# Performance work log

Measured on AMD Instinct MI355X. Metric: run time of the kernel, lower is better.

Reference implementation:

```python
import jax, jax.numpy as jnp
import numpy as np

N_LEVELS = 16
F_PER_LEVEL = 2
LOG2_T = 19
T = 1 << LOG2_T            # 524288 entries per level
BASE_RES = 16
PER_LEVEL_SCALE = 1.3819
HIDDEN = 64
DIM = 3
PRIMES = (1, 2654435761, 805459861)  # tcnn spatial hash primes

# 8 corner offsets of the unit cube, shape (8, 3)
_CORNERS = np.stack(np.meshgrid(*([np.array([0, 1])] * DIM), indexing='ij'), -1).reshape(-1, DIM)


def hashgrid_encode(x01, table):
    """x01: (N,3) in [0,1]; table: (L, T, F). Returns (N, L*F)."""
    offs = jnp.asarray(_CORNERS, dtype=jnp.int32)          # (8,3)
    offs_u = offs.astype(jnp.uint32)
    feats = []
    for lvl in range(N_LEVELS):
        scale = BASE_RES * (PER_LEVEL_SCALE ** lvl) - 1.0   # grid scale (tcnn convention)
        res = int(np.ceil(scale)) + 1                       # grid resolution for this level
        pos = x01 * jnp.float32(scale) + 0.5
        p0 = jnp.floor(pos)
        w = pos - p0                                        # (N,3) trilinear weights
        p0i = p0.astype(jnp.int32)
        corner = p0i[:, None, :] + offs[None]               # (N,8,3)
        if res ** DIM <= T:
            # dense (coarse) level: linear indexing
            idx = corner[..., 0] + corner[..., 1] * res + corner[..., 2] * (res * res)
        else:
            # fine level: xor spatial hash modulo table size
            c = p0i[:, None, :].astype(jnp.uint32) + offs_u[None]
            h = (c[..., 0] * jnp.uint32(PRIMES[0])) ^ (c[..., 1] * jnp.uint32(PRIMES[1])) ^ (c[..., 2] * jnp.uint32(PRIMES[2]))
            idx = (h & jnp.uint32(T - 1)).astype(jnp.int32)
        cf = table[lvl][idx]                                # (N,8,F) irregular gather
        # trilinear weight per corner: prod over dims of (w if offset==1 else 1-w)
        wmask = jnp.where(offs[None] == 1, w[:, None, :], 1.0 - w[:, None, :])  # (N,8,3)
        wc = jnp.prod(wmask, axis=-1)                       # (N,8)
        feats.append(jnp.sum(cf * wc[..., None], axis=1))   # (N,F)
    return jnp.concatenate(feats, axis=-1)                  # (N, 32)


def _xavier(key, fan_in, fan_out):
    lim = jnp.sqrt(6.0 / (fan_in + fan_out))
    return jax.random.uniform(key, (fan_in, fan_out), jnp.float32, -lim, lim)


def setup_inputs() -> dict:
    key = jax.random.key(0)
    k = jax.random.split(key, 8)
    x = jax.random.uniform(k[0], (1048576, DIM), jnp.float32, -1.0, 1.0)
    # tcnn hashgrid init: uniform(-1e-4, 1e-4)
    table = jax.random.uniform(k[1], (N_LEVELS, T, F_PER_LEVEL), jnp.float32, -1e-4, 1e-4)
    in_dim = N_LEVELS * F_PER_LEVEL
    W1 = _xavier(k[2], in_dim, HIDDEN); b1 = jnp.zeros((HIDDEN,), jnp.float32)
    W2 = _xavier(k[3], HIDDEN, HIDDEN); b2 = jnp.zeros((HIDDEN,), jnp.float32)
    W3 = _xavier(k[4], HIDDEN, 1);      b3 = jnp.zeros((1,), jnp.float32)
    return {"x": x, "table": table, "W1": W1, "b1": b1, "W2": W2, "b2": b2, "W3": W3, "b3": b3}


def reference(x, table, W1, b1, W2, b2, W3, b3):
    x01 = (x + 1.0) * 0.5                       # map [-1,1] -> [0,1]
    enc = hashgrid_encode(x01, table)           # (N, 32)
    h = jax.nn.relu(enc @ W1 + b1)
    h = jax.nn.relu(h @ W2 + b2)
    h = h @ W3 + b3                             # (N, 1), clip_sdf is None
    return h
```

## Files before the change

kernel.cpp:

```cpp
#include <hip/hip_runtime.h>
#include <hip/hip_fp16.h>
#include <cstdint>

#define NTHREADS 256
#define TBL_SIZE (1u << 19)
#define HIDDEN 64
#define NLVL 16
#define NDENSE 5
#define NHASH (NLVL - NDENSE)
#define PPT 2
#define ENC_SCALE 256.0f
#define ENC_INV (1.0f / 256.0f)

struct Levels { float scale[16]; int res[16]; int dense[16]; };
constexpr Levels make_levels() {
    Levels L{};
    double s = 16.0;
    for (int l = 0; l < 16; ++l) {
        double sc = s - 1.0;
        L.scale[l] = (float)sc;
        int fi = (int)sc;
        int res = fi + (((double)fi < sc) ? 1 : 0) + 1;
        L.res[l] = res;
        L.dense[l] = ((long long)res * res * res <= (long long)TBL_SIZE) ? 1 : 0;
        s *= 1.3819;
    }
    return L;
}
constexpr Levels LV = make_levels();
static_assert(LV.dense[NDENSE - 1] == 1 && LV.dense[NDENSE] == 0, "dense split");

struct PairOffs { int off[17]; int total; };
constexpr PairOffs make_pairoffs() {
    PairOffs P{}; int o = 0;
    for (int l = 0; l < 16; ++l) {
        P.off[l] = o;
        if (LV.dense[l]) {
            const int r = LV.res[l];
            o += r * (1 + r + r * r) + 2;
        }
    }
    P.off[16] = o; P.total = o;
    return P;
}
constexpr PairOffs PO = make_pairoffs();

#define H16(M) M(0) M(1) M(2) M(3) M(4) M(5) M(6) M(7) \
               M(8) M(9) M(10) M(11) M(12) M(13) M(14) M(15)

typedef _Float16 f16x8 __attribute__((ext_vector_type(8)));
typedef float f32x4 __attribute__((ext_vector_type(4)));

static __device__ __forceinline__ __half2 u32_h2(uint32_t u) {
    union { uint32_t u; __half2 h; } c; c.u = u; return c.h;
}
static __device__ __forceinline__ uint32_t h2_u32(__half2 h) {
    union { __half2 h; uint32_t u; } c; c.h = h; return c.u;
}

__global__ __launch_bounds__(256) void cvt_table(const float2* __restrict__ in,
                                                 __half2* __restrict__ out, int n) {
    for (int i = blockIdx.x * 256 + threadIdx.x; i < n; i += gridDim.x * 256) {
        const float2 v = in[i];
        out[i] = __floats2half2_rn(v.x, v.y);
    }
}

__global__ __launch_bounds__(256) void cvt_quads(const float2* __restrict__ tf,
                                                 uint4* __restrict__ qd) {
    for (int i = blockIdx.x * 256 + threadIdx.x; i < PO.total; i += gridDim.x * 256) {
        int lvl = 0;
        #pragma unroll
        for (int l = 0; l < NLVL; ++l)
            if (LV.dense[l] && i >= PO.off[l] && i < PO.off[l + 1]) lvl = l;
        const int local = i - PO.off[lvl];
        const int res = LV.res[lvl];
        const float2* base = tf + (size_t)lvl * TBL_SIZE + local;
        uint4 q;
        q.x = h2_u32(__floats2half2_rn(base[0].x, base[0].y));
        q.y = h2_u32(__floats2half2_rn(base[1].x, base[1].y));
        q.z = h2_u32(__floats2half2_rn(base[res].x, base[res].y));
        q.w = h2_u32(__floats2half2_rn(base[res + 1].x, base[res + 1].y));
        qd[i] = q;
    }
}

__global__ __launch_bounds__(256) void cvt_wfrags(const float* __restrict__ W1,
                                                  const float* __restrict__ W2,
                                                  __half* __restrict__ w1f,
                                                  __half* __restrict__ w2f) {
    const int t = blockIdx.x * 256 + threadIdx.x;
    for (int i = t; i < 4 * 64 * 8; i += gridDim.x * 256) {
        const int j = i & 7, lane = (i >> 3) & 63, nt = i >> 9;
        const int k = (lane >> 4) * 8 + j;
        const int o = (lane & 15) + 16 * nt;
        w1f[i] = __float2half(W1[k * HIDDEN + o]);
    }
    for (int i = t; i < 4 * 2 * 64 * 8; i += gridDim.x * 256) {
        const int j = i & 7, lane = (i >> 3) & 63, kb = (i >> 9) & 1, nt = i >> 10;
        const int k = 32 * kb + (lane >> 4) * 8 + j;
        const int o = (lane & 15) + 16 * nt;
        w2f[i] = __float2half(W2[k * HIDDEN + o]);
    }
}

static __device__ __forceinline__ float2 gather_dense(
    const uint4* __restrict__ qd, int res, int doff,
    int iu, int iv, int iw, float wu, float wv, float ww)
{
    float f0 = 0.0f, f1 = 0.0f;
    const float lx = 1.0f - wu;
    const int base = iu + iv * res + iw * res * res;
    #pragma unroll
    for (int o2 = 0; o2 < 2; ++o2) {
        const int idx = base + (o2 ? res * res : 0);
        const uint4 q = qd[doff + idx];
        const float2 a = __half22float2(u32_h2(q.x));
        const float2 b = __half22float2(u32_h2(q.y));
        const float2 c = __half22float2(u32_h2(q.z));
        const float2 d = __half22float2(u32_h2(q.w));
        const float x0l = fmaf(lx, a.x, wu * b.x);
        const float x1l = fmaf(lx, c.x, wu * d.x);
        const float y0l = fmaf(lx, a.y, wu * b.y);
        const float y1l = fmaf(lx, c.y, wu * d.y);
        const float bil0 = fmaf(1.0f - wv, x0l, wv * x1l);
        const float bil1 = fmaf(1.0f - wv, y0l, wv * y1l);
        const float wz = o2 ? ww : 1.0f - ww;
        f0 = fmaf(bil0, wz, f0);
        f1 = fmaf(bil1, wz, f1);
    }
    return make_float2(f0, f1);
}

static __device__ __forceinline__ float2 gather_hash(
    const __half2* __restrict__ tl,
    int iu, int iv, int iw, float wu, float wv, float ww)
{
    float f0 = 0.0f, f1 = 0.0f;
    const float lx = 1.0f - wu;
    const uint32_t r1a = (uint32_t)iv * 2654435761u;
    const uint32_t r1b = r1a + 2654435761u;
    const uint32_t r2a = (uint32_t)iw * 805459861u;
    const uint32_t r2b = r2a + 805459861u;
    if ((iu & 1) == 0) {
        #pragma unroll
        for (int b4 = 0; b4 < 4; ++b4) {
            const int o1 = (b4 >> 1) & 1, o2 = b4 & 1;
            const uint32_t rest = (o1 ? r1b : r1a) ^ (o2 ? r2b : r2a);
            const uint32_t h0 = ((uint32_t)iu ^ rest) & (TBL_SIZE - 1u);
            const unsigned long long pr =
                *reinterpret_cast<const unsigned long long*>(tl + (h0 & ~1u));
            const uint32_t lo = (uint32_t)pr, hi = (uint32_t)(pr >> 32);
            const uint32_t sel = h0 & 1u;
            const float2 a = __half22float2(u32_h2(sel ? hi : lo));
            const float2 b = __half22float2(u32_h2(sel ? lo : hi));
            const float wyz = (o1 ? wv : 1.0f - wv) * (o2 ? ww : 1.0f - ww);
            f0 = fmaf(fmaf(lx, a.x, wu * b.x), wyz, f0);
            f1 = fmaf(fmaf(lx, a.y, wu * b.y), wyz, f1);
        }
    } else {
        #pragma unroll
        for (int b4 = 0; b4 < 4; ++b4) {
            const int o1 = (b4 >> 1) & 1, o2 = b4 & 1;
            const uint32_t rest = (o1 ? r1b : r1a) ^ (o2 ? r2b : r2a);
            const uint32_t h0 = ((uint32_t)iu ^ rest) & (TBL_SIZE - 1u);
            const uint32_t h1 = ((uint32_t)(iu + 1) ^ rest) & (TBL_SIZE - 1u);
            const float2 a = __half22float2(tl[h0]);
            const float2 b = __half22float2(tl[h1]);
            const float wyz = (o1 ? wv : 1.0f - wv) * (o2 ? ww : 1.0f - ww);
            f0 = fmaf(fmaf(lx, a.x, wu * b.x), wyz, f0);
            f1 = fmaf(fmaf(lx, a.y, wu * b.y), wyz, f1);
        }
    }
    return make_float2(f0, f1);
}

__global__ __launch_bounds__(NTHREADS, 8) void encode_dense(
    const float* __restrict__ x,
    const uint4* __restrict__ qd,
    __half2* __restrict__ enc, int n)
{
    const int i0 = blockIdx.x * (NTHREADS * PPT) + threadIdx.x;
    const int i1 = i0 + NTHREADS;
    if (i0 >= n) return;

    const float u0 = (x[3 * i0 + 0] + 1.0f) * 0.5f;
    const float v0 = (x[3 * i0 + 1] + 1.0f) * 0.5f;
    const float w0 = (x[3 * i0 + 2] + 1.0f) * 0.5f;
    const bool has1 = (i1 < n);
    const int j1 = has1 ? i1 : i0;
    const float u1 = (x[3 * j1 + 0] + 1.0f) * 0.5f;
    const float v1 = (x[3 * j1 + 1] + 1.0f) * 0.5f;
    const float w1 = (x[3 * j1 + 2] + 1.0f) * 0.5f;

    #pragma unroll
    for (int l = 0; l < NDENSE; ++l) {
        const float sc = LV.scale[l];
        const int res = LV.res[l];
        const int doff = PO.off[l];

        const float pu0 = u0 * sc + 0.5f, pv0 = v0 * sc + 0.5f, pw0 = w0 * sc + 0.5f;
        const float fu0 = floorf(pu0), fv0 = floorf(pv0), fw0 = floorf(pw0);
        const float2 fA = gather_dense(qd, res, doff, (int)fu0, (int)fv0, (int)fw0,
                                       pu0 - fu0, pv0 - fv0, pw0 - fw0);
        const float pu1 = u1 * sc + 0.5f, pv1 = v1 * sc + 0.5f, pw1 = w1 * sc + 0.5f;
        const float fu1 = floorf(pu1), fv1 = floorf(pv1), fw1 = floorf(pw1);
        const float2 fB = gather_dense(qd, res, doff, (int)fu1, (int)fv1, (int)fw1,
                                       pu1 - fu1, pv1 - fv1, pw1 - fw1);

        enc[(size_t)l * n + i0] = __floats2half2_rn(fA.x * ENC_SCALE, fA.y * ENC_SCALE);
        if (has1) enc[(size_t)l * n + i1] = __floats2half2_rn(fB.x * ENC_SCALE, fB.y * ENC_SCALE);
    }
}

__global__ __launch_bounds__(NTHREADS, 8) void encode_hash(
    const float* __restrict__ x,
    const __half2* __restrict__ tbl,
    __half2* __restrict__ enc, int n, int nb)
{
    const int bid = blockIdx.x;
    const int lvl = NDENSE + bid / nb;
    const int pb  = bid - (lvl - NDENSE) * nb;
    const int i0 = pb * (NTHREADS * PPT) + threadIdx.x;
    const int i1 = i0 + NTHREADS;
    if (i0 >= n) return;

    const float sc = LV.scale[lvl];
    const __half2* tl = tbl + (size_t)lvl * TBL_SIZE;

    const float u0 = (x[3 * i0 + 0] + 1.0f) * 0.5f;
    const float v0 = (x[3 * i0 + 1] + 1.0f) * 0.5f;
    const float w0 = (x[3 * i0 + 2] + 1.0f) * 0.5f;
    const float pu0 = u0 * sc + 0.5f, pv0 = v0 * sc + 0.5f, pw0 = w0 * sc + 0.5f;
    const float fu0 = floorf(pu0), fv0 = floorf(pv0), fw0 = floorf(pw0);

    const bool has1 = (i1 < n);
    const int j1 = has1 ? i1 : i0;
    const float u1 = (x[3 * j1 + 0] + 1.0f) * 0.5f;
    const float v1 = (x[3 * j1 + 1] + 1.0f) * 0.5f;
    const float w1 = (x[3 * j1 + 2] + 1.0f) * 0.5f;
    const float pu1 = u1 * sc + 0.5f, pv1 = v1 * sc + 0.5f, pw1 = w1 * sc + 0.5f;
    const float fu1 = floorf(pu1), fv1 = floorf(pv1), fw1 = floorf(pw1);

    const float2 fA = gather_hash(tl, (int)fu0, (int)fv0, (int)fw0,
                                  pu0 - fu0, pv0 - fv0, pw0 - fw0);
    const float2 fB = gather_hash(tl, (int)fu1, (int)fv1, (int)fw1,
                                  pu1 - fu1, pv1 - fv1, pw1 - fw1);

    enc[(size_t)lvl * n + i0] = __floats2half2_rn(fA.x * ENC_SCALE, fA.y * ENC_SCALE);
    if (has1) enc[(size_t)lvl * n + i1] = __floats2half2_rn(fB.x * ENC_SCALE, fB.y * ENC_SCALE);
}

__global__ __launch_bounds__(256) void mlp_mfma(
    const __half2* __restrict__ enc,
    const __half* __restrict__ w1f, const __half* __restrict__ w2f,
    const float* __restrict__ b1, const float* __restrict__ b2,
    const float* __restrict__ W3, const float* __restrict__ b3,
    float* __restrict__ out, int n)
{
    __shared__ __half lds_h1[4][64][18];
    const int wid  = threadIdx.x >> 6;
    const int lane = threadIdx.x & 63;
    const int tile = blockIdx.x * 4 + wid;
    const int pt = lane & 15;
    const int qw = lane >> 4;
    const int i = tile * 16 + pt;

    union { uint32_t u[4]; f16x8 v; } bf;
    #pragma unroll
    for (int jj = 0; jj < 4; ++jj)
        bf.u[jj] = *reinterpret_cast<const uint32_t*>(&enc[(size_t)(qw * 4 + jj) * n + i]);

    f32x4 c1[4];
    #pragma unroll
    for (int nt = 0; nt < 4; ++nt) {
        const float4 bb = *(const float4*)&b1[16 * nt + qw * 4];
        c1[nt][0] = bb.x * ENC_SCALE; c1[nt][1] = bb.y * ENC_SCALE;
        c1[nt][2] = bb.z * ENC_SCALE; c1[nt][3] = bb.w * ENC_SCALE;
        const f16x8 a = *reinterpret_cast<const f16x8*>(&w1f[(nt * 64 + lane) * 8]);
        c1[nt] = __builtin_amdgcn_mfma_f32_16x16x32_f16(a, bf.v, c1[nt], 0, 0, 0);
    }

    #pragma unroll
    for (int nt = 0; nt < 4; ++nt) {
        #pragma unroll
        for (int r = 0; r < 4; ++r) {
            const int o = 16 * nt + qw * 4 + r;
            lds_h1[wid][o][pt] = __float2half(fmaxf(c1[nt][r], 0.0f));
        }
    }

    f32x4 c2[4];
    #pragma unroll
    for (int nt = 0; nt < 4; ++nt) {
        const float4 bb = *(const float4*)&b2[16 * nt + qw * 4];
        c2[nt][0] = bb.x * ENC_SCALE; c2[nt][1] = bb.y * ENC_SCALE;
        c2[nt][2] = bb.z * ENC_SCALE; c2[nt][3] = bb.w * ENC_SCALE;
    }
    #pragma unroll
    for (int kb = 0; kb < 2; ++kb) {
        union { uint32_t u[4]; f16x8 v; } hb;
        #pragma unroll
        for (int j2 = 0; j2 < 4; ++j2) {
            const int k0 = kb * 32 + qw * 8 + 2 * j2;
            const uint32_t lo = __half_as_ushort(lds_h1[wid][k0][pt]);
            const uint32_t hi = __half_as_ushort(lds_h1[wid][k0 + 1][pt]);
            hb.u[j2] = lo | (hi << 16);
        }
        #pragma unroll
        for (int nt = 0; nt < 4; ++nt) {
            const f16x8 a = *reinterpret_cast<const f16x8*>(&w2f[((nt * 2 + kb) * 64 + lane) * 8]);
            c2[nt] = __builtin_amdgcn_mfma_f32_16x16x32_f16(a, hb.v, c2[nt], 0, 0, 0);
        }
    }

    float part = 0.0f;
    #pragma unroll
    for (int nt = 0; nt < 4; ++nt) {
        const float4 w3v = *(const float4*)&W3[16 * nt + qw * 4];
        part = fmaf(fmaxf(c2[nt][0], 0.0f), w3v.x, part);
        part = fmaf(fmaxf(c2[nt][1], 0.0f), w3v.y, part);
        part = fmaf(fmaxf(c2[nt][2], 0.0f), w3v.z, part);
        part = fmaf(fmaxf(c2[nt][3], 0.0f), w3v.w, part);
    }
    part += __shfl_xor(part, 16, 64);
    part += __shfl_xor(part, 32, 64);
    if (lane < 16) out[i] = part * ENC_INV + b3[0];
}

template <bool USE_H2>
__global__ __launch_bounds__(NTHREADS, 4) void sdf_tcnn_fused(
    const float* __restrict__ x,
    const void* __restrict__ tbl,
    const float* __restrict__ W1, const float* __restrict__ b1,
    const float* __restrict__ W2, const float* __restrict__ b2,
    const float* __restrict__ W3, const float* __restrict__ b3,
    float* __restrict__ out, int n)
{
    const int i = blockIdx.x * NTHREADS + threadIdx.x;
    if (i >= n) return;

    const float u = (x[3 * i + 0] + 1.0f) * 0.5f;
    const float v = (x[3 * i + 1] + 1.0f) * 0.5f;
    const float w = (x[3 * i + 2] + 1.0f) * 0.5f;

#define DECLH(m) float4 h##m = *(const float4*)&b1[4 * (m)];
    H16(DECLH)
#undef DECLH

    #pragma unroll
    for (int l = 0; l < NLVL; ++l) {
        const float sc = LV.scale[l];
        const int res = LV.res[l];
        const float pu = u * sc + 0.5f;
        const float pv = v * sc + 0.5f;
        const float pw = w * sc + 0.5f;
        const float fu = floorf(pu), fv = floorf(pv), fw = floorf(pw);
        const float wu = pu - fu, wv = pv - fv, ww = pw - fw;
        const int iu = (int)fu, iv = (int)fv, iw = (int)fw;

        int idx[8];
        #pragma unroll
        for (int b = 0; b < 8; ++b) {
            const int o0 = (b >> 2) & 1, o1 = (b >> 1) & 1, o2 = b & 1;
            if (LV.dense[l]) {
                idx[b] = (iu + o0) + (iv + o1) * res + (iw + o2) * (res * res);
            } else {
                const uint32_t c0 = (uint32_t)(iu + o0);
                const uint32_t c1 = (uint32_t)(iv + o1);
                const uint32_t c2 = (uint32_t)(iw + o2);
                const uint32_t h = c0 ^ (c1 * 2654435761u) ^ (c2 * 805459861u);
                idx[b] = (int)(h & (TBL_SIZE - 1u));
            }
        }

        float f0 = 0.0f, f1 = 0.0f;
        if constexpr (USE_H2) {
            const __half2* tl = (const __half2*)tbl + (size_t)l * TBL_SIZE;
            __half2 cfh[8];
            #pragma unroll
            for (int b = 0; b < 8; ++b) cfh[b] = tl[idx[b]];
            #pragma unroll
            for (int b = 0; b < 8; ++b) {
                const int o0 = (b >> 2) & 1, o1 = (b >> 1) & 1, o2 = b & 1;
                const float wt = (o0 ? wu : 1.0f - wu) *
                                 (o1 ? wv : 1.0f - wv) *
                                 (o2 ? ww : 1.0f - ww);
                const float2 cf = __half22float2(cfh[b]);
                f0 = fmaf(cf.x, wt, f0);
                f1 = fmaf(cf.y, wt, f1);
            }
        } else {
            const float2* tl = (const float2*)tbl + (size_t)l * TBL_SIZE;
            float2 cf[8];
            #pragma unroll
            for (int b = 0; b < 8; ++b) cf[b] = tl[idx[b]];
            #pragma unroll
            for (int b = 0; b < 8; ++b) {
                const int o0 = (b >> 2) & 1, o1 = (b >> 1) & 1, o2 = b & 1;
                const float wt = (o0 ? wu : 1.0f - wu) *
                                 (o1 ? wv : 1.0f - wv) *
                                 (o2 ? ww : 1.0f - ww);
                f0 = fmaf(cf[b].x, wt, f0);
                f1 = fmaf(cf[b].y, wt, f1);
            }
        }

        const float* wra = &W1[(2 * l) * HIDDEN];
        const float* wrb = &W1[(2 * l + 1) * HIDDEN];
#define UPDH(m) { \
        const float4 wa = *(const float4*)&wra[4 * (m)]; \
        const float4 wb = *(const float4*)&wrb[4 * (m)]; \
        h##m.x = fmaf(f0, wa.x, fmaf(f1, wb.x, h##m.x)); \
        h##m.y = fmaf(f0, wa.y, fmaf(f1, wb.y, h##m.y)); \
        h##m.z = fmaf(f0, wa.z, fmaf(f1, wb.z, h##m.z)); \
        h##m.w = fmaf(f0, wa.w, fmaf(f1, wb.w, h##m.w)); }
        H16(UPDH)
#undef UPDH
    }

#define RELUH(m) { h##m.x = fmaxf(h##m.x, 0.0f); h##m.y = fmaxf(h##m.y, 0.0f); \
                   h##m.z = fmaxf(h##m.z, 0.0f); h##m.w = fmaxf(h##m.w, 0.0f); }
    H16(RELUH)
#undef RELUH

    float acc = b3[0];
    #pragma unroll 2
    for (int jb = 0; jb < HIDDEN; jb += 4) {
        float4 t = *(const float4*)&b2[jb];
#define L2K(m) { \
        const float4 r0 = *(const float4*)&W2[(4 * (m) + 0) * HIDDEN + jb]; \
        const float4 r1 = *(const float4*)&W2[(4 * (m) + 1) * HIDDEN + jb]; \
        const float4 r2 = *(const float4*)&W2[(4 * (m) + 2) * HIDDEN + jb]; \
        const float4 r3 = *(const float4*)&W2[(4 * (m) + 3) * HIDDEN + jb]; \
        t.x = fmaf(h##m.x, r0.x, t.x); t.y = fmaf(h##m.x, r0.y, t.y); \
        t.z = fmaf(h##m.x, r0.z, t.z); t.w = fmaf(h##m.x, r0.w, t.w); \
        t.x = fmaf(h##m.y, r1.x, t.x); t.y = fmaf(h##m.y, r1.y, t.y); \
        t.z = fmaf(h##m.y, r1.z, t.z); t.w = fmaf(h##m.y, r1.w, t.w); \
        t.x = fmaf(h##m.z, r2.x, t.x); t.y = fmaf(h##m.z, r2.y, t.y); \
        t.z = fmaf(h##m.z, r2.z, t.z); t.w = fmaf(h##m.z, r2.w, t.w); \
        t.x = fmaf(h##m.w, r3.x, t.x); t.y = fmaf(h##m.w, r3.y, t.y); \
        t.z = fmaf(h##m.w, r3.z, t.z); t.w = fmaf(h##m.w, r3.w, t.w); }
        H16(L2K)
#undef L2K
        const float4 w3v = *(const float4*)&W3[jb];
        acc = fmaf(fmaxf(t.x, 0.0f), w3v.x, acc);
        acc = fmaf(fmaxf(t.y, 0.0f), w3v.y, acc);
        acc = fmaf(fmaxf(t.z, 0.0f), w3v.z, acc);
        acc = fmaf(fmaxf(t.w, 0.0f), w3v.w, acc);
    }

    out[i] = acc;
}

extern "C" void kernel_launch(void* const* d_in, const int* in_sizes, int n_in,
                              void* d_out, int out_size, void* d_ws, size_t ws_size,
                              hipStream_t stream) {
    const float* x     = (const float*)d_in[0];
    const float* table = (const float*)d_in[1];
    const float* W1    = (const float*)d_in[2];
    const float* b1    = (const float*)d_in[3];
    const float* W2    = (const float*)d_in[4];
    const float* b2    = (const float*)d_in[5];
    const float* W3    = (const float*)d_in[6];
    const float* b3    = (const float*)d_in[7];
    float* out = (float*)d_out;

    const int n = in_sizes[0] / 3;
    const int n_entries = NLVL * (int)TBL_SIZE;
    const size_t tbl_bytes   = (size_t)n_entries * sizeof(__half2);
    const size_t quad_bytes  = (size_t)PO.total * 16;
    const size_t wfrag_bytes = 16384;
    const size_t enc_bytes   = (size_t)NLVL * (size_t)n * sizeof(__half2);
    const int nb_mlp = (n + NTHREADS - 1) / NTHREADS;
    const int nb_enc = (n + NTHREADS * PPT - 1) / (NTHREADS * PPT);

    if (ws_size >= tbl_bytes + quad_bytes + wfrag_bytes + enc_bytes) {
        __half2* tbl_h2 = (__half2*)d_ws;
        uint4* qd = (uint4*)((char*)d_ws + tbl_bytes);
        __half* w1f = (__half*)((char*)d_ws + tbl_bytes + quad_bytes);
        __half* w2f = w1f + 4 * 64 * 8;
        __half2* enc = (__half2*)((char*)d_ws + tbl_bytes + quad_bytes + wfrag_bytes);

        hipLaunchKernelGGL(cvt_table, dim3(2048), dim3(256), 0, stream,
                           (const float2*)table + (size_t)NDENSE * TBL_SIZE,
                           tbl_h2 + (size_t)NDENSE * TBL_SIZE,
                           NHASH * (int)TBL_SIZE);
        hipLaunchKernelGGL(cvt_quads, dim3((PO.total + 255) / 256), dim3(256), 0, stream,
                           (const float2*)table, qd);
        hipLaunchKernelGGL(cvt_wfrags, dim3(16), dim3(256), 0, stream,
                           W1, W2, w1f, w2f);
        hipLaunchKernelGGL(encode_dense, dim3(nb_enc), dim3(NTHREADS), 0, stream,
                           x, qd, enc, n);
        hipLaunchKernelGGL(encode_hash, dim3(nb_enc * NHASH), dim3(NTHREADS), 0, stream,
                           x, tbl_h2, enc, n, nb_enc);
        hipLaunchKernelGGL(mlp_mfma, dim3((n + 63) / 64), dim3(256), 0, stream,
                           enc, w1f, w2f, b1, b2, W3, b3, out, n);
    } else {
        hipLaunchKernelGGL((sdf_tcnn_fused<false>), dim3(nb_mlp), dim3(NTHREADS), 0, stream,
                           x, (const void*)table, W1, b1, W2, b2, W3, b3, out, n);
    }
}
```

Baseline: 321.1 us.

## Fuse conversion kernels, densify first hashed level, multi-tile MLP waves

Merges the three preprocessing kernels into one cvt_all launch. Level 5 (the first hashed level, whose grid only slightly exceeds the table size) gets a precomputed dense quad table, so its lookups use the coalesced dense gather instead of 8 hashed reads. The MLP kernel now keeps weight fragments and biases in registers and processes 4 tiles per wave, which cuts repeated weight loads at the cost of register pressure. The qd5 path adds workspace and precompute work and needs enough workspace to be enabled.

```diff
diff --git a/kernel.cpp b/kernel.cpp
--- a/kernel.cpp
+++ b/kernel.cpp
@@ -11,6 +11,7 @@
 #define PPT 2
 #define ENC_SCALE 256.0f
 #define ENC_INV (1.0f / 256.0f)
+#define MLP_TPW 4
 
 struct Levels { float scale[16]; int res[16]; int dense[16]; };
 constexpr Levels make_levels() {
@@ -45,6 +46,9 @@
 }
 constexpr PairOffs PO = make_pairoffs();
 
+constexpr int RES5 = LV.res[NDENSE];
+constexpr int QD5_TOTAL = RES5 * (1 + RES5 + RES5 * RES5) + 2;
+
 #define H16(M) M(0) M(1) M(2) M(3) M(4) M(5) M(6) M(7) \
                M(8) M(9) M(10) M(11) M(12) M(13) M(14) M(15)
 
@@ -57,22 +61,32 @@
 static __device__ __forceinline__ uint32_t h2_u32(__half2 h) {
     union { __half2 h; uint32_t u; } c; c.h = h; return c.u;
 }
-
-__global__ __launch_bounds__(256) void cvt_table(const float2* __restrict__ in,
-                                                 __half2* __restrict__ out, int n) {
-    for (int i = blockIdx.x * 256 + threadIdx.x; i < n; i += gridDim.x * 256) {
-        const float2 v = in[i];
-        out[i] = __floats2half2_rn(v.x, v.y);
-    }
-}
-
-__global__ __launch_bounds__(256) void cvt_quads(const float2* __restrict__ tf,
-                                                 uint4* __restrict__ qd) {
-    for (int i = blockIdx.x * 256 + threadIdx.x; i < PO.total; i += gridDim.x * 256) {
+static __device__ __forceinline__ uint32_t hash3(uint32_t c0, uint32_t c1, uint32_t c2) {
+    return (c0 ^ (c1 * 2654435761u) ^ (c2 * 805459861u)) & (TBL_SIZE - 1u);
+}
+
+__global__ __launch_bounds__(256) void cvt_all(
+    const float2* __restrict__ tf, __half2* __restrict__ tbl_h2,
+    uint4* __restrict__ qd, uint4* __restrict__ qd5,
+    const float* __restrict__ W1, const float* __restrict__ W2,
+    __half* __restrict__ w1f, __half* __restrict__ w2f, int use_qd5)
+{
+    const int gid = blockIdx.x * 256 + threadIdx.x;
+    const int stride = gridDim.x * 256;
+
+    const int W_tbl = NHASH * (int)TBL_SIZE;
+    const float2* tf_h = tf + (size_t)NDENSE * TBL_SIZE;
+    __half2* th_h = tbl_h2 + (size_t)NDENSE * TBL_SIZE;
+    for (int i = gid; i < W_tbl; i += stride) {
+        const float2 v = tf_h[i];
+        th_h[i] = __floats2half2_rn(v.x, v.y);
+    }
+
+    for (int i = gid; i < PO.total; i += stride) {
         int lvl = 0;
         #pragma unroll
-        for (int l = 0; l < NLVL; ++l)
-            if (LV.dense[l] && i >= PO.off[l] && i < PO.off[l + 1]) lvl = l;
+        for (int l = 0; l < NDENSE; ++l)
+            if (i >= PO.off[l] && i < PO.off[l + 1]) lvl = l;
         const int local = i - PO.off[lvl];
         const int res = LV.res[lvl];
         const float2* base = tf + (size_t)lvl * TBL_SIZE + local;
@@ -83,20 +97,34 @@
         q.w = h2_u32(__floats2half2_rn(base[res + 1].x, base[res + 1].y));
         qd[i] = q;
     }
-}
-
-__global__ __launch_bounds__(256) void cvt_wfrags(const float* __restrict__ W1,
-                                                  const float* __restrict__ W2,
-                                                  __half* __restrict__ w1f,
-                                                  __half* __restrict__ w2f) {
-    const int t = blockIdx.x * 256 + threadIdx.x;
-    for (int i = t; i < 4 * 64 * 8; i += gridDim.x * 256) {
+
+    if (use_qd5) {
+        const float2* t5 = tf + (size_t)NDENSE * TBL_SIZE;
+        for (int i = gid; i < QD5_TOTAL; i += stride) {
+            const uint32_t c2 = (uint32_t)i / (uint32_t)(RES5 * RES5);
+            const uint32_t rem = (uint32_t)i % (uint32_t)(RES5 * RES5);
+            const uint32_t c1 = rem / (uint32_t)RES5;
+            const uint32_t c0 = rem % (uint32_t)RES5;
+            const float2 a = t5[hash3(c0, c1, c2)];
+            const float2 b = t5[hash3(c0 + 1, c1, c2)];
+            const float2 c = t5[hash3(c0, c1 + 1, c2)];
+            const float2 d = t5[hash3(c0 + 1, c1 + 1, c2)];
+            uint4 q;
+            q.x = h2_u32(__floats2half2_rn(a.x, a.y));
+            q.y = h2_u32(__floats2half2_rn(b.x, b.y));
+            q.z = h2_u32(__floats2half2_rn(c.x, c.y));
+            q.w = h2_u32(__floats2half2_rn(d.x, d.y));
+            qd5[i] = q;
+        }
+    }
+
+    for (int i = gid; i < 4 * 64 * 8; i += stride) {
         const int j = i & 7, lane = (i >> 3) & 63, nt = i >> 9;
         const int k = (lane >> 4) * 8 + j;
         const int o = (lane & 15) + 16 * nt;
         w1f[i] = __float2half(W1[k * HIDDEN + o]);
     }
-    for (int i = t; i < 4 * 2 * 64 * 8; i += gridDim.x * 256) {
+    for (int i = gid; i < 4 * 2 * 64 * 8; i += stride) {
         const int j = i & 7, lane = (i >> 3) & 63, kb = (i >> 9) & 1, nt = i >> 10;
         const int k = 32 * kb + (lane >> 4) * 8 + j;
         const int o = (lane & 15) + 16 * nt;
@@ -216,6 +244,7 @@
 __global__ __launch_bounds__(NTHREADS, 8) void encode_hash(
     const float* __restrict__ x,
     const __half2* __restrict__ tbl,
+    const uint4* __restrict__ qd5, int use_qd5,
     __half2* __restrict__ enc, int n, int nb)
 {
     const int bid = blockIdx.x;
@@ -242,16 +271,24 @@
     const float pu1 = u1 * sc + 0.5f, pv1 = v1 * sc + 0.5f, pw1 = w1 * sc + 0.5f;
     const float fu1 = floorf(pu1), fv1 = floorf(pv1), fw1 = floorf(pw1);
 
-    const float2 fA = gather_hash(tl, (int)fu0, (int)fv0, (int)fw0,
-                                  pu0 - fu0, pv0 - fv0, pw0 - fw0);
-    const float2 fB = gather_hash(tl, (int)fu1, (int)fv1, (int)fw1,
-                                  pu1 - fu1, pv1 - fv1, pw1 - fw1);
+    float2 fA, fB;
+    if (lvl == NDENSE && use_qd5) {
+        fA = gather_dense(qd5, RES5, 0, (int)fu0, (int)fv0, (int)fw0,
+                          pu0 - fu0, pv0 - fv0, pw0 - fw0);
+        fB = gather_dense(qd5, RES5, 0, (int)fu1, (int)fv1, (int)fw1,
+                          pu1 - fu1, pv1 - fv1, pw1 - fw1);
+    } else {
+        fA = gather_hash(tl, (int)fu0, (int)fv0, (int)fw0,
+                         pu0 - fu0, pv0 - fv0, pw0 - fw0);
+        fB = gather_hash(tl, (int)fu1, (int)fv1, (int)fw1,
+                         pu1 - fu1, pv1 - fv1, pw1 - fw1);
+    }
 
     enc[(size_t)lvl * n + i0] = __floats2half2_rn(fA.x * ENC_SCALE, fA.y * ENC_SCALE);
     if (has1) enc[(size_t)lvl * n + i1] = __floats2half2_rn(fB.x * ENC_SCALE, fB.y * ENC_SCALE);
 }
 
-__global__ __launch_bounds__(256) void mlp_mfma(
+__global__ __launch_bounds__(256, 3) void mlp_mfma(
     const __half2* __restrict__ enc,
     const __half* __restrict__ w1f, const __half* __restrict__ w2f,
     const float* __restrict__ b1, const float* __restrict__ b2,
@@ -261,77 +298,96 @@
     __shared__ __half lds_h1[4][64][18];
     const int wid  = threadIdx.x >> 6;
     const int lane = threadIdx.x & 63;
-    const int tile = blockIdx.x * 4 + wid;
     const int pt = lane & 15;
     const int qw = lane >> 4;
-    const int i = tile * 16 + pt;
-
-    union { uint32_t u[4]; f16x8 v; } bf;
-    #pragma unroll
-    for (int jj = 0; jj < 4; ++jj)
-        bf.u[jj] = *reinterpret_cast<const uint32_t*>(&enc[(size_t)(qw * 4 + jj) * n + i]);
-
-    f32x4 c1[4];
+
+    f16x8 a1[4];
+    #pragma unroll
+    for (int nt = 0; nt < 4; ++nt)
+        a1[nt] = *reinterpret_cast<const f16x8*>(&w1f[(nt * 64 + lane) * 8]);
+    f16x8 a2[8];
+    #pragma unroll
+    for (int q8 = 0; q8 < 8; ++q8)
+        a2[q8] = *reinterpret_cast<const f16x8*>(&w2f[(q8 * 64 + lane) * 8]);
+
+    float4 bb1[4], bb2[4], w3v[4];
     #pragma unroll
     for (int nt = 0; nt < 4; ++nt) {
-        const float4 bb = *(const float4*)&b1[16 * nt + qw * 4];
-        c1[nt][0] = bb.x * ENC_SCALE; c1[nt][1] = bb.y * ENC_SCALE;
-        c1[nt][2] = bb.z * ENC_SCALE; c1[nt][3] = bb.w * ENC_SCALE;
-        const f16x8 a = *reinterpret_cast<const f16x8*>(&w1f[(nt * 64 + lane) * 8]);
-        c1[nt] = __builtin_amdgcn_mfma_f32_16x16x32_f16(a, bf.v, c1[nt], 0, 0, 0);
-    }
-
-    #pragma unroll
-    for (int nt = 0; nt < 4; ++nt) {
-        #pragma unroll
-        for (int r = 0; r < 4; ++r) {
-            const int o = 16 * nt + qw * 4 + r;
-            lds_h1[wid][o][pt] = __float2half(fmaxf(c1[nt][r], 0.0f));
-        }
-    }
-
-    f32x4 c2[4];
-    #pragma unroll
-    for (int nt = 0; nt < 4; ++nt) {
-        const float4 bb = *(const float4*)&b2[16 * nt + qw * 4];
-        c2[nt][0] = bb.x * ENC_SCALE; c2[nt][1] = bb.y * ENC_SCALE;
-        c2[nt][2] = bb.z * ENC_SCALE; c2[nt][3] = bb.w * ENC_SCALE;
-    }
-    #pragma unroll
-    for (int kb = 0; kb < 2; ++kb) {
-        union { uint32_t u[4]; f16x8 v; } hb;
-        #pragma unroll
-        for (int j2 = 0; j2 < 4; ++j2) {
-            const int k0 = kb * 32 + qw * 8 + 2 * j2;
-            const uint32_t lo = __half_as_ushort(lds_h1[wid][k0][pt]);
-            const uint32_t hi = __half_as_ushort(lds_h1[wid][k0 + 1][pt]);
-            hb.u[j2] = lo | (hi << 16);
-        }
+        const float4 t1 = *(const float4*)&b1[16 * nt + qw * 4];
+        bb1[nt] = make_float4(t1.x * ENC_SCALE, t1.y * ENC_SCALE, t1.z * ENC_SCALE, t1.w * ENC_SCALE);
+        const float4 t2 = *(const float4*)&b2[16 * nt + qw * 4];
+        bb2[nt] = make_float4(t2.x * ENC_SCALE, t2.y * ENC_SCALE, t2.z * ENC_SCALE, t2.w * ENC_SCALE);
+        w3v[nt] = *(const float4*)&W3[16 * nt + qw * 4];
+    }
+    const float b3s = b3[0];
+
+    const int base_tile = (blockIdx.x * 4 + wid) * MLP_TPW;
+
+    #pragma unroll
+    for (int t = 0; t < MLP_TPW; ++t) {
+        const int i = (base_tile + t) * 16 + pt;
+        const int ic = (i < n) ? i : (n - 1);
+
+        union { uint32_t u[4]; f16x8 v; } bf;
+        #pragma unroll
+        for (int jj = 0; jj < 4; ++jj)
+            bf.u[jj] = *reinterpret_cast<const uint32_t*>(&enc[(size_t)(qw * 4 + jj) * n + ic]);
+
+        f32x4 c1[4];
         #pragma unroll
         for (int nt = 0; nt < 4; ++nt) {
-            const f16x8 a = *reinterpret_cast<const f16x8*>(&w2f[((nt * 2 + kb) * 64 + lane) * 8]);
-            c2[nt] = __builtin_amdgcn_mfma_f32_16x16x32_f16(a, hb.v, c2[nt], 0, 0, 0);
-        }
-    }
-
-    float part = 0.0f;
-    #pragma unroll
-    for (int nt = 0; nt < 4; ++nt) {
-        const float4 w3v = *(const float4*)&W3[16 * nt + qw * 4];
-        part = fmaf(fmaxf(c2[nt][0], 0.0f), w3v.x, part);
-        part = fmaf(fmaxf(c2[nt][1], 0.0f), w3v.y, part);
-        part = fmaf(fmaxf(c2[nt][2], 0.0f), w3v.z, part);
-        part = fmaf(fmaxf(c2[nt][3], 0.0f), w3v.w, part);
-    }
-    part += __shfl_xor(part, 16, 64);
-    part += __shfl_xor(part, 32, 64);
-    if (lane < 16) out[i] = part * ENC_INV + b3[0];
-}
-
-template <bool USE_H2>
+            c1[nt][0] = bb1[nt].x; c1[nt][1] = bb1[nt].y;
+            c1[nt][2] = bb1[nt].z; c1[nt][3] = bb1[nt].w;
+            c1[nt] = __builtin_amdgcn_mfma_f32_16x16x32_f16(a1[nt], bf.v, c1[nt], 0, 0, 0);
+        }
+
+        #pragma unroll
+        for (int nt = 0; nt < 4; ++nt) {
+            #pragma unroll
+            for (int r = 0; r < 4; ++r) {
+                const int o = 16 * nt + qw * 4 + r;
+                lds_h1[wid][o][pt] = __float2half(fmaxf(c1[nt][r], 0.0f));
+            }
+        }
+
+        f32x4 c2[4];
+        #pragma unroll
+        for (int nt = 0; nt < 4; ++nt) {
+            c2[nt][0] = bb2[nt].x; c2[nt][1] = bb2[nt].y;
+            c2[nt][2] = bb2[nt].z; c2[nt][3] = bb2[nt].w;
+        }
+        #pragma unroll
+        for (int kb = 0; kb < 2; ++kb) {
+            union { uint32_t u[4]; f16x8 v; } hb;
+            #pragma unroll
+            for (int j2 = 0; j2 < 4; ++j2) {
+                const int k0 = kb * 32 + qw * 8 + 2 * j2;
+                const uint32_t lo = __half_as_ushort(lds_h1[wid][k0][pt]);
+                const uint32_t hi = __half_as_ushort(lds_h1[wid][k0 + 1][pt]);
+                hb.u[j2] = lo | (hi << 16);
+            }
+            #pragma unroll
+            for (int nt = 0; nt < 4; ++nt)
+                c2[nt] = __builtin_amdgcn_mfma_f32_16x16x32_f16(a2[nt * 2 + kb], hb.v, c2[nt], 0, 0, 0);
+        }
+
+        float part = 0.0f;
+        #pragma unroll
+        for (int nt = 0; nt < 4; ++nt) {
+            part = fmaf(fmaxf(c2[nt][0], 0.0f), w3v[nt].x, part);
+            part = fmaf(fmaxf(c2[nt][1], 0.0f), w3v[nt].y, part);
+            part = fmaf(fmaxf(c2[nt][2], 0.0f), w3v[nt].z, part);
+            part = fmaf(fmaxf(c2[nt][3], 0.0f), w3v[nt].w, part);
+        }
+        part += __shfl_xor(part, 16, 64);
+        part += __shfl_xor(part, 32, 64);
+        if (lane < 16 && i < n) out[i] = part * ENC_INV + b3s;
+    }
+}
+
 __global__ __launch_bounds__(NTHREADS, 4) void sdf_tcnn_fused(
     const float* __restrict__ x,
-    const void* __restrict__ tbl,
+    const float* __restrict__ tblf,
     const float* __restrict__ W1, const float* __restrict__ b1,
     const float* __restrict__ W2, const float* __restrict__ b2,
     const float* __restrict__ W3, const float* __restrict__ b3,
@@ -366,44 +422,22 @@
             if (LV.dense[l]) {
                 idx[b] = (iu + o0) + (iv + o1) * res + (iw + o2) * (res * res);
             } else {
-                const uint32_t c0 = (uint32_t)(iu + o0);
-                const uint32_t c1 = (uint32_t)(iv + o1);
-                const uint32_t c2 = (uint32_t)(iw + o2);
-                const uint32_t h = c0 ^ (c1 * 2654435761u) ^ (c2 * 805459861u);
-                idx[b] = (int)(h & (TBL_SIZE - 1u));
+                idx[b] = (int)hash3((uint32_t)(iu + o0), (uint32_t)(iv + o1), (uint32_t)(iw + o2));
             }
         }
-
+        const float2* tl = (const float2*)tblf + (size_t)l * TBL_SIZE;
+        float2 cf[8];
+        #pragma unroll
+        for (int b = 0; b < 8; ++b) cf[b] = tl[idx[b]];
         float f0 = 0.0f, f1 = 0.0f;
-        if constexpr (USE_H2) {
-            const __half2* tl = (const __half2*)tbl + (size_t)l * TBL_SIZE;
-            __half2 cfh[8];
-            #pragma unroll
-            for (int b = 0; b < 8; ++b) cfh[b] = tl[idx[b]];
-            #pragma unroll
-            for (int b = 0; b < 8; ++b) {
-                const int o0 = (b >> 2) & 1, o1 = (b >> 1) & 1, o2 = b & 1;
-                const float wt = (o0 ? wu : 1.0f - wu) *
-                                 (o1 ? wv : 1.0f - wv) *
-                                 (o2 ? ww : 1.0f - ww);
-                const float2 cf = __half22float2(cfh[b]);
-                f0 = fmaf(cf.x, wt, f0);
-                f1 = fmaf(cf.y, wt, f1);
-            }
-        } else {
-            const float2* tl = (const float2*)tbl + (size_t)l * TBL_SIZE;
-            float2 cf[8];
-            #pragma unroll
-            for (int b = 0; b < 8; ++b) cf[b] = tl[idx[b]];
-            #pragma unroll
-            for (int b = 0; b < 8; ++b) {
-                const int o0 = (b >> 2) & 1, o1 = (b >> 1) & 1, o2 = b & 1;
-                const float wt = (o0 ? wu : 1.0f - wu) *
-                                 (o1 ? wv : 1.0f - wv) *
-                                 (o2 ? ww : 1.0f - ww);
-                f0 = fmaf(cf[b].x, wt, f0);
-                f1 = fmaf(cf[b].y, wt, f1);
-            }
+        #pragma unroll
+        for (int b = 0; b < 8; ++b) {
+            const int o0 = (b >> 2) & 1, o1 = (b >> 1) & 1, o2 = b & 1;
+            const float wt = (o0 ? wu : 1.0f - wu) *
+                             (o1 ? wv : 1.0f - wv) *
+                             (o2 ? ww : 1.0f - ww);
+            f0 = fmaf(cf[b].x, wt, f0);
+            f1 = fmaf(cf[b].y, wt, f1);
         }
 
         const float* wra = &W1[(2 * l) * HIDDEN];
@@ -467,37 +501,35 @@
     float* out = (float*)d_out;
 
     const int n = in_sizes[0] / 3;
-    const int n_entries = NLVL * (int)TBL_SIZE;
-    const size_t tbl_bytes   = (size_t)n_entries * sizeof(__half2);
+    const size_t tbl_bytes   = (size_t)NLVL * TBL_SIZE * sizeof(__half2);
     const size_t quad_bytes  = (size_t)PO.total * 16;
+    const size_t qd5_bytes   = (size_t)QD5_TOTAL * 16;
     const size_t wfrag_bytes = 16384;
     const size_t enc_bytes   = (size_t)NLVL * (size_t)n * sizeof(__half2);
-    const int nb_mlp = (n + NTHREADS - 1) / NTHREADS;
+    const size_t base_need   = tbl_bytes + quad_bytes + wfrag_bytes + enc_bytes;
     const int nb_enc = (n + NTHREADS * PPT - 1) / (NTHREADS * PPT);
 
-    if (ws_size >= tbl_bytes + quad_bytes + wfrag_bytes + enc_bytes) {
-        __half2* tbl_h2 = (__half2*)d_ws;
-        uint4* qd = (uint4*)((char*)d_ws + tbl_bytes);
-        __half* w1f = (__half*)((char*)d_ws + tbl_bytes + quad_bytes);
-        __half* w2f = w1f + 4 * 64 * 8;
-        __half2* enc = (__half2*)((char*)d_ws + tbl_bytes + quad_bytes + wfrag_bytes);
-
-        hipLaunchKernelGGL(cvt_table, dim3(2048), dim3(256), 0, stream,
-                           (const float2*)table + (size_t)NDENSE * TBL_SIZE,
-                           tbl_h2 + (size_t)NDENSE * TBL_SIZE,
-                           NHASH * (int)TBL_SIZE);
-        hipLaunchKernelGGL(cvt_quads, dim3((PO.total + 255) / 256), dim3(256), 0, stream,
-                           (const float2*)table, qd);
-        hipLaunchKernelGGL(cvt_wfrags, dim3(16), dim3(256), 0, stream,
-                           W1, W2, w1f, w2f);
+    if (ws_size >= base_need) {
+        const int use_qd5 = (ws_size >= base_need + qd5_bytes) ? 1 : 0;
+        char* p = (char*)d_ws;
+        __half2* tbl_h2 = (__half2*)p;                 p += tbl_bytes;
+        uint4* qd = (uint4*)p;                         p += quad_bytes;
+        __half* w1f = (__half*)p;                      p += 4 * 64 * 8 * sizeof(__half);
+        __half* w2f = (__half*)p;                      p += 4 * 2 * 64 * 8 * sizeof(__half);
+        __half2* enc = (__half2*)p;                    p += enc_bytes;
+        uint4* qd5 = use_qd5 ? (uint4*)p : nullptr;
+
+        hipLaunchKernelGGL(cvt_all, dim3(4096), dim3(256), 0, stream,
+                           (const float2*)table, tbl_h2, qd, qd5, W1, W2, w1f, w2f, use_qd5);
         hipLaunchKernelGGL(encode_dense, dim3(nb_enc), dim3(NTHREADS), 0, stream,
                            x, qd, enc, n);
         hipLaunchKernelGGL(encode_hash, dim3(nb_enc * NHASH), dim3(NTHREADS), 0, stream,
-                           x, tbl_h2, enc, n, nb_enc);
-        hipLaunchKernelGGL(mlp_mfma, dim3((n + 63) / 64), dim3(256), 0, stream,
+                           x, tbl_h2, qd5, use_qd5, enc, n, nb_enc);
+        hipLaunchKernelGGL(mlp_mfma, dim3((n + 16 * MLP_TPW * 4 - 1) / (16 * MLP_TPW * 4)),
+                           dim3(256), 0, stream,
                            enc, w1f, w2f, b1, b2, W3, b3, out, n);
     } else {
-        hipLaunchKernelGGL((sdf_tcnn_fused<false>), dim3(nb_mlp), dim3(NTHREADS), 0, stream,
-                           x, (const void*)table, W1, b1, W2, b2, W3, b3, out, n);
-    }
-}
+        hipLaunchKernelGGL(sdf_tcnn_fused, dim3((n + NTHREADS - 1) / NTHREADS), dim3(NTHREADS), 0, stream,
+                           x, table, W1, b1, W2, b2, W3, b3, out, n);
+    }
+}
```

Result: faster. 307.5 us (-4.2%).
